# Kernel optimization log

Hardware: AMD Instinct MI355X
Metric: run time of the kernel (lower is better)

Reference implementation:

```python
import jax, jax.numpy as jnp
import numpy as np

N_NODES = 50000
N_EDGES = 1600000
E_DIM = 128
N_LAYERS = 3
N_GRAPHS = 32


def setup_inputs() -> dict:
    key = jax.random.key(0)
    ks = jax.random.split(key, 12)
    x = jax.random.normal(ks[0], (N_NODES,), dtype=jnp.float32)
    edge_index = jax.random.randint(ks[1], (2, N_EDGES), 0, N_NODES, dtype=jnp.int32)
    batch = jnp.sort(jax.random.randint(ks[2], (N_NODES,), 0, N_GRAPHS, dtype=jnp.int32))
    s_in = 1.0  # fan_in = 1 for the first linear
    s_e = 1.0 / np.sqrt(E_DIM)
    lin_w = jax.random.normal(ks[3], (1, E_DIM), jnp.float32) * s_in
    lin_b = jax.random.normal(ks[4], (E_DIM,), jnp.float32) * 0.01
    gcn_w = jax.random.normal(ks[5], (N_LAYERS, E_DIM, E_DIM), jnp.float32) * s_e
    gcn_b = jax.random.normal(ks[6], (N_LAYERS, E_DIM), jnp.float32) * 0.01
    r1_w = jax.random.normal(ks[7], (E_DIM, E_DIM), jnp.float32) * s_e
    r1_b = jax.random.normal(ks[8], (E_DIM,), jnp.float32) * 0.01
    r2_w = jax.random.normal(ks[9], (E_DIM, 1), jnp.float32) * s_e
    r2_b = jax.random.normal(ks[10], (1,), jnp.float32) * 0.01
    return {"x": x, "edge_index": edge_index, "batch": batch,
            "lin_w": lin_w, "lin_b": lin_b, "gcn_w": gcn_w, "gcn_b": gcn_b,
            "r1_w": r1_w, "r1_b": r1_b, "r2_w": r2_w, "r2_b": r2_b}


def reference(x, edge_index, batch, lin_w, lin_b, gcn_w, gcn_b, r1_w, r1_b, r2_w, r2_b):
    # input embedding: x.view(-1, 1) @ W + b -> [N, E]
    h = x.reshape(-1, 1) @ lin_w + lin_b

    # GCN normalization (add self-loops, symmetric deg^-1/2 norm) — structure is
    # identical across layers, so compute once.
    loops = jnp.arange(N_NODES, dtype=edge_index.dtype)
    src = jnp.concatenate([edge_index[0], loops])
    dst = jnp.concatenate([edge_index[1], loops])
    deg = jax.ops.segment_sum(jnp.ones(src.shape[0], h.dtype), dst, num_segments=N_NODES)
    dinv = jnp.where(deg > 0, jax.lax.rsqrt(deg), 0.0)
    norm = (dinv[src] * dinv[dst])[:, None]  # [E+N, 1]

    # NOTE: original calls x.relu() without assignment -> no activation (faithful).
    for l in range(N_LAYERS):
        h = h @ gcn_w[l]                                        # [N, E]
        h = jax.ops.segment_sum(h[src] * norm, dst, num_segments=N_NODES) + gcn_b[l]

    # global_add_pool over graphs
    pooled = jax.ops.segment_sum(h, batch, num_segments=N_GRAPHS)  # [G, E]
    hr = jnp.tanh(pooled @ r1_w + r1_b)
    return hr @ r2_w + r2_b  # [G, 1]
```

## Files before the change

kernel.cpp:

```cpp
#include <hip/hip_runtime.h>
#include <hip/hip_bf16.h>
#include <math.h>

#define NGRAPH 32
#define CAP 10240
#define EPT 24
#define EPB (256 * EPT)

__global__ void k_part(const int* __restrict__ src, const int* __restrict__ dst,
                       int* __restrict__ gcursor, unsigned int* __restrict__ packed, int E) {
    __shared__ unsigned int ldsbuf[EPB];
    __shared__ int hist[256], lofs[256], lcur[256], base[256];
    int tid = threadIdx.x;
    int e0 = blockIdx.x * EPB;
    hist[tid] = 0;
    __syncthreads();
    int d[EPT], s[EPT];
#pragma unroll
    for (int c = 0; c < EPT / 4; c++) {
        int e = e0 + c * 1024 + (tid << 2);
        if (e + 3 < E) {
            int4 dv = *(const int4*)&dst[e];
            int4 sv = *(const int4*)&src[e];
            d[4*c+0] = dv.x; d[4*c+1] = dv.y; d[4*c+2] = dv.z; d[4*c+3] = dv.w;
            s[4*c+0] = sv.x; s[4*c+1] = sv.y; s[4*c+2] = sv.z; s[4*c+3] = sv.w;
            atomicAdd(&hist[dv.x >> 8], 1);
            atomicAdd(&hist[dv.y >> 8], 1);
            atomicAdd(&hist[dv.z >> 8], 1);
            atomicAdd(&hist[dv.w >> 8], 1);
        } else {
#pragma unroll
            for (int k = 0; k < 4; k++) {
                int ee = e + k;
                if (ee < E) {
                    d[4*c+k] = dst[ee]; s[4*c+k] = src[ee];
                    atomicAdd(&hist[d[4*c+k] >> 8], 1);
                } else {
                    d[4*c+k] = -1;
                }
            }
        }
    }
    __syncthreads();
    int v = hist[tid];
    lofs[tid] = v;
    __syncthreads();
    for (int off = 1; off < 256; off <<= 1) {
        int t = (tid >= off) ? lofs[tid - off] : 0;
        __syncthreads();
        lofs[tid] += t;
        __syncthreads();
    }
    int total = lofs[255];
    int excl = lofs[tid] - v;
    lofs[tid] = excl;
    lcur[tid] = excl;
    if (v > 0) base[tid] = tid * CAP + atomicAdd(&gcursor[tid], v);
    __syncthreads();
#pragma unroll
    for (int c = 0; c < EPT; c++) {
        int dd = d[c];
        if (dd >= 0) {
            int bk = dd >> 8;
            int slot = atomicAdd(&lcur[bk], 1);
            ldsbuf[slot] = ((unsigned int)bk << 24) | ((unsigned int)s[c] << 8)
                         | (unsigned int)(dd & 255);
        }
    }
    __syncthreads();
    for (int i = tid; i < total; i += 256) {
        unsigned int w = ldsbuf[i];
        int bk = w >> 24;
        packed[base[bk] + (i - lofs[bk])] = w & 0xFFFFFFu;
    }
}

__global__ void k_bucket(const unsigned int* __restrict__ packed, const int* __restrict__ gcursor,
                         const float* __restrict__ x, const int* __restrict__ batch,
                         int* __restrict__ offs, int* __restrict__ deg,
                         float* __restrict__ dinv, float2* __restrict__ q0,
                         unsigned short* __restrict__ csr, float* __restrict__ S, int N) {
    __shared__ int cnt[256], lofs[256], lcur[256];
    __shared__ float cs[NGRAPH];
    int tid = threadIdx.x;
    int b = blockIdx.x;
    int start = b * CAP;
    int end = start + gcursor[b];
    cnt[tid] = 0;
    if (tid < NGRAPH) cs[tid] = 0.f;
    __syncthreads();
    for (int e = start + tid; e < end; e += 256)
        atomicAdd(&cnt[packed[e] & 255], 1);
    __syncthreads();
    int v = cnt[tid];
    int vp = (v + 1) & ~1;
    lofs[tid] = vp;
    __syncthreads();
    for (int off = 1; off < 256; off <<= 1) {
        int t = (tid >= off) ? lofs[tid - off] : 0;
        __syncthreads();
        lofs[tid] += t;
        __syncthreads();
    }
    int excl = lofs[tid] - vp;
    lcur[tid] = excl;
    int node = b * 256 + tid;
    if (node < N) {
        deg[node] = v;
        offs[node] = start + excl;
        float dv = rsqrtf((float)(v + 1));
        dinv[node] = dv;
        q0[node] = make_float2(x[node] * dv, dv);
        atomicAdd(&cs[batch[node]], 1.f);
    }
    __syncthreads();
    for (int e = start + tid; e < end; e += 256) {
        unsigned int p = packed[e];
        int pos = start + atomicAdd(&lcur[p & 255], 1);
        csr[pos] = (unsigned short)(p >> 8);
    }
    if (tid < NGRAPH && cs[tid] != 0.f) atomicAdd(&S[tid], cs[tid]);
}

template <int WRITE_Q>
__global__ void k_hop(const float2* __restrict__ qin, float2* __restrict__ outv,
                      const unsigned short* __restrict__ csr,
                      const int* __restrict__ offs, const int* __restrict__ deg,
                      const float* __restrict__ dinv, int N) {
    int tid = threadIdx.x;
    int lane = tid & 15;
    int node = blockIdx.x * 16 + (tid >> 4);
    if (node >= N) return;
    int e = offs[node], ne = deg[node];
    float sx = 0.0f, su = 0.0f;
    for (int j = 2 * lane; j < ne; j += 32) {
        ushort2 c = *(const ushort2*)&csr[e + j];
        float2 a = qin[c.x];
        sx += a.x; su += a.y;
        if (j + 1 < ne) {
            float2 b = qin[c.y];
            sx += b.x; su += b.y;
        }
    }
#pragma unroll
    for (int m = 8; m > 0; m >>= 1) {
        sx += __shfl_xor(sx, m);
        su += __shfl_xor(su, m);
    }
    if (lane == 0) {
        float2 qs = qin[node];
        float dv = dinv[node];
        float px = dv * (sx + qs.x), pu = dv * (su + qs.y);
        if (WRITE_Q) outv[node] = make_float2(px * dv, pu * dv);
        else         outv[node] = make_float2(px, pu);
    }
}

__global__ __launch_bounds__(1024) void k_chain(
        const float* __restrict__ lin_w, const float* __restrict__ lin_b,
        const float* __restrict__ gcn_w, const float* __restrict__ gcn_b,
        float* __restrict__ chainv) {
    __shared__ float W[128 * 128];
    __shared__ float v4[4 * 128];
    __shared__ float part[4 * 128 * 8];
    int tid = threadIdx.x;
    int j = tid & 127;
    int ch = tid >> 7;
    if (tid < 128) {
        v4[tid]       = lin_w[tid];
        v4[128 + tid] = lin_b[tid];
        v4[256 + tid] = gcn_b[tid];
        v4[384 + tid] = gcn_b[128 + tid];
    }
    for (int l = 0; l < 3; l++) {
        __syncthreads();
        const float4* Wg = (const float4*)(gcn_w + l * 128 * 128);
        float4* Ws = (float4*)W;
#pragma unroll
        for (int i = 0; i < 4; i++) Ws[tid + i * 1024] = Wg[tid + i * 1024];
        __syncthreads();
        float na = 0.f, nb = 0.f, nc = 0.f, nd = 0.f;
#pragma unroll
        for (int kk = 0; kk < 16; kk++) {
            int k = ch * 16 + kk;
            float w = W[k * 128 + j];
            na += v4[k] * w;
            nb += v4[128 + k] * w;
            nc += v4[256 + k] * w;
            nd += v4[384 + k] * w;
        }
        part[(0 * 128 + j) * 8 + ch] = na;
        part[(1 * 128 + j) * 8 + ch] = nb;
        part[(2 * 128 + j) * 8 + ch] = nc;
        part[(3 * 128 + j) * 8 + ch] = nd;
        __syncthreads();
        if (tid < 512) {
            int vec = tid >> 7, jj = tid & 127;
            float s = 0.f;
#pragma unroll
            for (int c = 0; c < 8; c++) s += part[(vec * 128 + jj) * 8 + c];
            if (vec < 2 || (vec == 2 && l >= 1) || (vec == 3 && l >= 2))
                v4[vec * 128 + jj] = s;
        }
    }
    __syncthreads();
    if (tid < 512) chainv[tid] = v4[tid];
}

__global__ __launch_bounds__(256) void k_mlp(
        const float* __restrict__ S, const float* __restrict__ chainv,
        const float2* __restrict__ q1, const float2* __restrict__ q2,
        const float2* __restrict__ p3, const float* __restrict__ dinv,
        const float* __restrict__ gcn_b,
        const float* __restrict__ r1_w, const float* __restrict__ r1_b,
        const float* __restrict__ r2_w, const float* __restrict__ r2_b,
        float* __restrict__ out, int N) {
    __shared__ float rw[128 * 128];
    __shared__ float pl[128], red[128];
    __shared__ float cnts[NGRAPH];
    __shared__ float r4[4 * 128];
    int tid = threadIdx.x;
    int g = blockIdx.x;
    {
        const float4* Rg = (const float4*)r1_w;
        float4* Rs = (float4*)rw;
#pragma unroll
        for (int i = 0; i < 16; i++) Rs[tid + i * 256] = Rg[tid + i * 256];
    }
    if (tid < NGRAPH) cnts[tid] = S[tid];
    __syncthreads();
    int r0 = 0;
    for (int i = 0; i < g; i++) r0 += (int)cnts[i];
    int cnt = (int)cnts[g];
    int r1 = r0 + cnt;
    float su1 = 0.f, su2 = 0.f, su3 = 0.f, sv3 = 0.f;
    for (int n = r0 + tid; n < r1; n += 256) {
        float inv = 1.0f / dinv[n];
        su1 += q1[n].y * inv;
        su2 += q2[n].y * inv;
        float2 p = p3[n];
        su3 += p.y; sv3 += p.x;
    }
#pragma unroll
    for (int m = 32; m > 0; m >>= 1) {
        su1 += __shfl_xor(su1, m);
        su2 += __shfl_xor(su2, m);
        su3 += __shfl_xor(su3, m);
        sv3 += __shfl_xor(sv3, m);
    }
    int wv = tid >> 6;
    if ((tid & 63) == 0) {
        r4[wv] = su1; r4[4 + wv] = su2; r4[8 + wv] = su3; r4[12 + wv] = sv3;
    }
    __syncthreads();
    su1 = r4[0] + r4[1] + r4[2] + r4[3];
    su2 = r4[4] + r4[5] + r4[6] + r4[7];
    su3 = r4[8] + r4[9] + r4[10] + r4[11];
    sv3 = r4[12] + r4[13] + r4[14] + r4[15];
    const float* b3 = gcn_b + 2 * 128;
    if (tid < 128)
        pl[tid] = sv3 * chainv[tid] + su3 * chainv[128 + tid] + su2 * chainv[256 + tid]
                + su1 * chainv[384 + tid] + (float)cnt * b3[tid];
    __syncthreads();
    int j = tid & 127, half = tid >> 7;
    float acc = 0.f;
#pragma unroll
    for (int kk = 0; kk < 64; kk++) {
        int k = half * 64 + kk;
        acc += pl[k] * rw[k * 128 + j];
    }
    r4[half * 128 + j] = acc;
    __syncthreads();
    if (tid < 128) {
        float a = r4[tid] + r4[128 + tid] + r1_b[tid];
        red[tid] = tanhf(a) * r2_w[tid];
    }
    __syncthreads();
    for (int sft = 64; sft > 0; sft >>= 1) {
        if (tid < sft) red[tid] += red[tid + sft];
        __syncthreads();
    }
    if (tid == 0) out[g] = red[0] + r2_b[0];
}

extern "C" void kernel_launch(void* const* d_in, const int* in_sizes, int n_in,
                              void* d_out, int out_size, void* d_ws, size_t ws_size,
                              hipStream_t stream) {
    const float* x     = (const float*)d_in[0];
    const int*   eidx  = (const int*)d_in[1];
    const int*   batch = (const int*)d_in[2];
    const float* lin_w = (const float*)d_in[3];
    const float* lin_b = (const float*)d_in[4];
    const float* gcn_w = (const float*)d_in[5];
    const float* gcn_b = (const float*)d_in[6];
    const float* r1_w  = (const float*)d_in[7];
    const float* r1_b  = (const float*)d_in[8];
    const float* r2_w  = (const float*)d_in[9];
    const float* r2_b  = (const float*)d_in[10];

    const int N = in_sizes[0];
    const int E = in_sizes[1] / 2;
    const int* src = eidx;
    const int* dst = eidx + E;
    const int NB = (N + 255) / 256;

    char* w = (char*)d_ws;
    float2* q0      = (float2*)w; w += (size_t)N * 8;
    float2* q1      = (float2*)w; w += (size_t)N * 8;
    float2* q2      = (float2*)w; w += (size_t)N * 8;
    float2* p3      = (float2*)w; w += (size_t)N * 8;
    unsigned int* packed = (unsigned int*)w; w += (size_t)256 * CAP * 4;
    int*    offs    = (int*)w;    w += (size_t)N * 4;
    int*    deg     = (int*)w;    w += (size_t)N * 4;
    float*  dinv    = (float*)w;  w += (size_t)N * 4;
    int*    gcursor = (int*)w;    w += 256 * 4;
    float*  S       = (float*)w;  w += 64 * 4;
    float*  chainv  = (float*)w;  w += 512 * 4;
    unsigned short* csr = (unsigned short*)w; w += (size_t)256 * CAP * 2 + 256;

    hipMemsetAsync(gcursor, 0, 256 * 4 + 64 * 4, stream);

    k_part<<<(E + EPB - 1) / EPB, 256, 0, stream>>>(src, dst, gcursor, packed, E);
    k_bucket<<<NB, 256, 0, stream>>>(packed, gcursor, x, batch, offs, deg, dinv, q0, csr, S, N);

    int hop_blocks = (N + 15) / 16;
    k_hop<1><<<hop_blocks, 256, 0, stream>>>(q0, q1, csr, offs, deg, dinv, N);
    k_hop<1><<<hop_blocks, 256, 0, stream>>>(q1, q2, csr, offs, deg, dinv, N);
    k_hop<0><<<hop_blocks, 256, 0, stream>>>(q2, p3, csr, offs, deg, dinv, N);

    k_chain<<<1, 1024, 0, stream>>>(lin_w, lin_b, gcn_w, gcn_b, chainv);
    k_mlp<<<NGRAPH, 256, 0, stream>>>(S, chainv, q1, q2, p3, dinv, gcn_b,
                                      r1_w, r1_b, r2_w, r2_b, (float*)d_out, N);
}
```

Baseline: 165.7 us.

## Fuse all stages into one cooperative persistent kernel with grid syncs

Replaces seven separate launches plus a memset with a single cooperative kernel of 256 blocks of 1024 threads. Stages are separated by grid.sync(): partitioning, bucketing/CSR build with the weight chain computed by a spare block, three hop passes looping over node tiles, and the per-graph MLP. The aim is to remove per-launch overhead and the gaps between small kernels. In exchange, each stage now runs on a fixed 256-block grid instead of a grid sized to its work, the weight matrices are read straight from global memory rather than staged in LDS, and every stage pays for a grid barrier.

```diff
diff --git a/kernel.cpp b/kernel.cpp
--- a/kernel.cpp
+++ b/kernel.cpp
@@ -1,286 +1,305 @@
 #include <hip/hip_runtime.h>
-#include <hip/hip_bf16.h>
+#include <hip/hip_cooperative_groups.h>
 #include <math.h>
+
+namespace cg = cooperative_groups;
 
 #define NGRAPH 32
 #define CAP 10240
-#define EPT 24
-#define EPB (256 * EPT)
-
-__global__ void k_part(const int* __restrict__ src, const int* __restrict__ dst,
-                       int* __restrict__ gcursor, unsigned int* __restrict__ packed, int E) {
+#define BT 1024
+#define GRID 256
+#define EPT 8
+#define EPB (BT * EPT)
+
+__global__ __launch_bounds__(BT, 4) void k_fused(
+    const int* __restrict__ src, const int* __restrict__ dst,
+    const float* __restrict__ x, const int* __restrict__ batch,
+    const float* __restrict__ lin_w, const float* __restrict__ lin_b,
+    const float* __restrict__ gcn_w, const float* __restrict__ gcn_b,
+    const float* __restrict__ r1_w, const float* __restrict__ r1_b,
+    const float* __restrict__ r2_w, const float* __restrict__ r2_b,
+    float* __restrict__ out,
+    unsigned int* __restrict__ packed, unsigned short* __restrict__ csr,
+    int* __restrict__ offs, int* __restrict__ deg,
+    float* __restrict__ dinv, float2* __restrict__ q0, float2* __restrict__ q1,
+    float2* __restrict__ q2, float2* __restrict__ p3,
+    int* __restrict__ gcursor, float* __restrict__ S, float* __restrict__ chainv,
+    int N, int E)
+{
+    cg::grid_group grid = cg::this_grid();
     __shared__ unsigned int ldsbuf[EPB];
-    __shared__ int hist[256], lofs[256], lcur[256], base[256];
-    int tid = threadIdx.x;
-    int e0 = blockIdx.x * EPB;
-    hist[tid] = 0;
-    __syncthreads();
-    int d[EPT], s[EPT];
-#pragma unroll
-    for (int c = 0; c < EPT / 4; c++) {
-        int e = e0 + c * 1024 + (tid << 2);
-        if (e + 3 < E) {
-            int4 dv = *(const int4*)&dst[e];
-            int4 sv = *(const int4*)&src[e];
-            d[4*c+0] = dv.x; d[4*c+1] = dv.y; d[4*c+2] = dv.z; d[4*c+3] = dv.w;
-            s[4*c+0] = sv.x; s[4*c+1] = sv.y; s[4*c+2] = sv.z; s[4*c+3] = sv.w;
-            atomicAdd(&hist[dv.x >> 8], 1);
-            atomicAdd(&hist[dv.y >> 8], 1);
-            atomicAdd(&hist[dv.z >> 8], 1);
-            atomicAdd(&hist[dv.w >> 8], 1);
-        } else {
-#pragma unroll
-            for (int k = 0; k < 4; k++) {
-                int ee = e + k;
-                if (ee < E) {
-                    d[4*c+k] = dst[ee]; s[4*c+k] = src[ee];
-                    atomicAdd(&hist[d[4*c+k] >> 8], 1);
-                } else {
-                    d[4*c+k] = -1;
+    __shared__ int h0[256], h1[256], h2[256], h3[256];
+    __shared__ float fbuf[640];
+
+    const int tid = threadIdx.x;
+    const int b = blockIdx.x;
+    const int NB = (N + 255) >> 8;
+    const int ntiles = (E + EPB - 1) / EPB;
+    const int nvb = (N + 63) >> 6;
+
+    if (b == 0) {
+        if (tid < 256) gcursor[tid] = 0;
+        else if (tid < 320) S[tid - 256] = 0.f;
+    }
+    grid.sync();
+
+    if (b < ntiles) {
+        int e0 = b * EPB;
+        if (tid < 256) h0[tid] = 0;
+        __syncthreads();
+        int d[EPT], s[EPT];
+#pragma unroll
+        for (int c = 0; c < EPT / 4; c++) {
+            int e = e0 + c * 4096 + (tid << 2);
+            if (e + 3 < E) {
+                int4 dv = *(const int4*)&dst[e];
+                int4 sv = *(const int4*)&src[e];
+                d[4*c+0] = dv.x; d[4*c+1] = dv.y; d[4*c+2] = dv.z; d[4*c+3] = dv.w;
+                s[4*c+0] = sv.x; s[4*c+1] = sv.y; s[4*c+2] = sv.z; s[4*c+3] = sv.w;
+                atomicAdd(&h0[dv.x >> 8], 1);
+                atomicAdd(&h0[dv.y >> 8], 1);
+                atomicAdd(&h0[dv.z >> 8], 1);
+                atomicAdd(&h0[dv.w >> 8], 1);
+            } else {
+#pragma unroll
+                for (int k = 0; k < 4; k++) {
+                    int ee = e + k;
+                    if (ee < E) {
+                        d[4*c+k] = dst[ee]; s[4*c+k] = src[ee];
+                        atomicAdd(&h0[d[4*c+k] >> 8], 1);
+                    } else {
+                        d[4*c+k] = -1;
+                    }
                 }
             }
         }
-    }
-    __syncthreads();
-    int v = hist[tid];
-    lofs[tid] = v;
-    __syncthreads();
-    for (int off = 1; off < 256; off <<= 1) {
-        int t = (tid >= off) ? lofs[tid - off] : 0;
-        __syncthreads();
-        lofs[tid] += t;
-        __syncthreads();
-    }
-    int total = lofs[255];
-    int excl = lofs[tid] - v;
-    lofs[tid] = excl;
-    lcur[tid] = excl;
-    if (v > 0) base[tid] = tid * CAP + atomicAdd(&gcursor[tid], v);
-    __syncthreads();
-#pragma unroll
-    for (int c = 0; c < EPT; c++) {
-        int dd = d[c];
-        if (dd >= 0) {
-            int bk = dd >> 8;
-            int slot = atomicAdd(&lcur[bk], 1);
-            ldsbuf[slot] = ((unsigned int)bk << 24) | ((unsigned int)s[c] << 8)
-                         | (unsigned int)(dd & 255);
-        }
-    }
-    __syncthreads();
-    for (int i = tid; i < total; i += 256) {
-        unsigned int w = ldsbuf[i];
-        int bk = w >> 24;
-        packed[base[bk] + (i - lofs[bk])] = w & 0xFFFFFFu;
-    }
-}
-
-__global__ void k_bucket(const unsigned int* __restrict__ packed, const int* __restrict__ gcursor,
-                         const float* __restrict__ x, const int* __restrict__ batch,
-                         int* __restrict__ offs, int* __restrict__ deg,
-                         float* __restrict__ dinv, float2* __restrict__ q0,
-                         unsigned short* __restrict__ csr, float* __restrict__ S, int N) {
-    __shared__ int cnt[256], lofs[256], lcur[256];
-    __shared__ float cs[NGRAPH];
-    int tid = threadIdx.x;
-    int b = blockIdx.x;
-    int start = b * CAP;
-    int end = start + gcursor[b];
-    cnt[tid] = 0;
-    if (tid < NGRAPH) cs[tid] = 0.f;
-    __syncthreads();
-    for (int e = start + tid; e < end; e += 256)
-        atomicAdd(&cnt[packed[e] & 255], 1);
-    __syncthreads();
-    int v = cnt[tid];
-    int vp = (v + 1) & ~1;
-    lofs[tid] = vp;
-    __syncthreads();
-    for (int off = 1; off < 256; off <<= 1) {
-        int t = (tid >= off) ? lofs[tid - off] : 0;
-        __syncthreads();
-        lofs[tid] += t;
-        __syncthreads();
-    }
-    int excl = lofs[tid] - vp;
-    lcur[tid] = excl;
-    int node = b * 256 + tid;
-    if (node < N) {
-        deg[node] = v;
-        offs[node] = start + excl;
-        float dv = rsqrtf((float)(v + 1));
-        dinv[node] = dv;
-        q0[node] = make_float2(x[node] * dv, dv);
-        atomicAdd(&cs[batch[node]], 1.f);
-    }
-    __syncthreads();
-    for (int e = start + tid; e < end; e += 256) {
-        unsigned int p = packed[e];
-        int pos = start + atomicAdd(&lcur[p & 255], 1);
-        csr[pos] = (unsigned short)(p >> 8);
-    }
-    if (tid < NGRAPH && cs[tid] != 0.f) atomicAdd(&S[tid], cs[tid]);
-}
-
-template <int WRITE_Q>
-__global__ void k_hop(const float2* __restrict__ qin, float2* __restrict__ outv,
-                      const unsigned short* __restrict__ csr,
-                      const int* __restrict__ offs, const int* __restrict__ deg,
-                      const float* __restrict__ dinv, int N) {
-    int tid = threadIdx.x;
-    int lane = tid & 15;
-    int node = blockIdx.x * 16 + (tid >> 4);
-    if (node >= N) return;
-    int e = offs[node], ne = deg[node];
-    float sx = 0.0f, su = 0.0f;
-    for (int j = 2 * lane; j < ne; j += 32) {
-        ushort2 c = *(const ushort2*)&csr[e + j];
-        float2 a = qin[c.x];
-        sx += a.x; su += a.y;
-        if (j + 1 < ne) {
-            float2 b = qin[c.y];
-            sx += b.x; su += b.y;
-        }
-    }
-#pragma unroll
-    for (int m = 8; m > 0; m >>= 1) {
-        sx += __shfl_xor(sx, m);
-        su += __shfl_xor(su, m);
-    }
-    if (lane == 0) {
-        float2 qs = qin[node];
-        float dv = dinv[node];
-        float px = dv * (sx + qs.x), pu = dv * (su + qs.y);
-        if (WRITE_Q) outv[node] = make_float2(px * dv, pu * dv);
-        else         outv[node] = make_float2(px, pu);
-    }
-}
-
-__global__ __launch_bounds__(1024) void k_chain(
-        const float* __restrict__ lin_w, const float* __restrict__ lin_b,
-        const float* __restrict__ gcn_w, const float* __restrict__ gcn_b,
-        float* __restrict__ chainv) {
-    __shared__ float W[128 * 128];
-    __shared__ float v4[4 * 128];
-    __shared__ float part[4 * 128 * 8];
-    int tid = threadIdx.x;
-    int j = tid & 127;
-    int ch = tid >> 7;
-    if (tid < 128) {
-        v4[tid]       = lin_w[tid];
-        v4[128 + tid] = lin_b[tid];
-        v4[256 + tid] = gcn_b[tid];
-        v4[384 + tid] = gcn_b[128 + tid];
-    }
+        __syncthreads();
+        int v = 0;
+        if (tid < 256) { v = h0[tid]; h1[tid] = v; }
+        __syncthreads();
+        for (int off = 1; off < 256; off <<= 1) {
+            int t = 0;
+            if (tid < 256 && tid >= off) t = h1[tid - off];
+            __syncthreads();
+            if (tid < 256) h1[tid] += t;
+            __syncthreads();
+        }
+        int total = h1[255];
+        __syncthreads();
+        if (tid < 256) {
+            int excl = h1[tid] - v;
+            h1[tid] = excl;
+            h2[tid] = excl;
+            if (v > 0) h3[tid] = tid * CAP + atomicAdd(&gcursor[tid], v);
+        }
+        __syncthreads();
+#pragma unroll
+        for (int c = 0; c < EPT; c++) {
+            int dd = d[c];
+            if (dd >= 0) {
+                int bk = dd >> 8;
+                int slot = atomicAdd(&h2[bk], 1);
+                ldsbuf[slot] = ((unsigned int)bk << 24) | ((unsigned int)s[c] << 8)
+                             | (unsigned int)(dd & 255);
+            }
+        }
+        __syncthreads();
+        for (int i = tid; i < total; i += BT) {
+            unsigned int wv = ldsbuf[i];
+            int bk = wv >> 24;
+            packed[h3[bk] + (i - h1[bk])] = wv & 0xFFFFFFu;
+        }
+    }
+    grid.sync();
+
+    if (b < NB) {
+        int start = b * CAP;
+        int end = start + gcursor[b];
+        if (tid < 256) h0[tid] = 0;
+        if (tid < NGRAPH) fbuf[tid] = 0.f;
+        __syncthreads();
+        for (int e = start + tid; e < end; e += BT)
+            atomicAdd(&h0[packed[e] & 255], 1);
+        __syncthreads();
+        int v = 0, vp = 0;
+        if (tid < 256) {
+            v = h0[tid];
+            vp = (v + 1) & ~1;
+            h1[tid] = vp;
+        }
+        __syncthreads();
+        for (int off = 1; off < 256; off <<= 1) {
+            int t = 0;
+            if (tid < 256 && tid >= off) t = h1[tid - off];
+            __syncthreads();
+            if (tid < 256) h1[tid] += t;
+            __syncthreads();
+        }
+        if (tid < 256) {
+            int excl = h1[tid] - vp;
+            h2[tid] = excl;
+            int node = b * 256 + tid;
+            if (node < N) {
+                deg[node] = v;
+                offs[node] = start + excl;
+                float dv = rsqrtf((float)(v + 1));
+                dinv[node] = dv;
+                q0[node] = make_float2(x[node] * dv, dv);
+                atomicAdd(&fbuf[batch[node]], 1.f);
+            }
+        }
+        __syncthreads();
+        for (int e = start + tid; e < end; e += BT) {
+            unsigned int p = packed[e];
+            int pos = start + atomicAdd(&h2[p & 255], 1);
+            csr[pos] = (unsigned short)(p >> 8);
+        }
+        if (tid < NGRAPH && fbuf[tid] != 0.f) atomicAdd(&S[tid], fbuf[tid]);
+    } else if (b == NB) {
+        float* v4 = fbuf;
+        float* ch = (float*)ldsbuf;
+        if (tid < 128) {
+            v4[tid]       = lin_w[tid];
+            v4[128 + tid] = lin_b[tid];
+            v4[256 + tid] = gcn_b[tid];
+            v4[384 + tid] = gcn_b[128 + tid];
+        }
+        int j = tid & 127, kh = tid >> 7;
+        for (int l = 0; l < 3; l++) {
+            __syncthreads();
+            const float* W = gcn_w + l * 128 * 128;
+            float na = 0.f, nb = 0.f, nc = 0.f, nd = 0.f;
+#pragma unroll
+            for (int kk = 0; kk < 16; kk++) {
+                int k = kh * 16 + kk;
+                float w = W[k * 128 + j];
+                na += v4[k] * w;
+                nb += v4[128 + k] * w;
+                nc += v4[256 + k] * w;
+                nd += v4[384 + k] * w;
+            }
+            ch[(0 * 128 + j) * 8 + kh] = na;
+            ch[(1 * 128 + j) * 8 + kh] = nb;
+            ch[(2 * 128 + j) * 8 + kh] = nc;
+            ch[(3 * 128 + j) * 8 + kh] = nd;
+            __syncthreads();
+            if (tid < 512) {
+                int vec = tid >> 7, jj = tid & 127;
+                float s = 0.f;
+#pragma unroll
+                for (int c = 0; c < 8; c++) s += ch[(vec * 128 + jj) * 8 + c];
+                if (vec < 2 || (vec == 2 && l >= 1) || (vec == 3 && l >= 2))
+                    v4[vec * 128 + jj] = s;
+            }
+        }
+        __syncthreads();
+        if (tid < 512) chainv[tid] = v4[tid];
+    }
+    grid.sync();
+
+#pragma unroll
     for (int l = 0; l < 3; l++) {
-        __syncthreads();
-        const float4* Wg = (const float4*)(gcn_w + l * 128 * 128);
-        float4* Ws = (float4*)W;
-#pragma unroll
-        for (int i = 0; i < 4; i++) Ws[tid + i * 1024] = Wg[tid + i * 1024];
-        __syncthreads();
-        float na = 0.f, nb = 0.f, nc = 0.f, nd = 0.f;
+        const float2* qin = (l == 0) ? q0 : (l == 1) ? q1 : q2;
+        float2* outv      = (l == 0) ? q1 : (l == 1) ? q2 : p3;
+        int lane = tid & 15;
+        int sub = tid >> 4;
+        for (int vb = b; vb < nvb; vb += GRID) {
+            int node = vb * 64 + sub;
+            if (node < N) {
+                int e = offs[node], ne = deg[node];
+                float sx = 0.f, su = 0.f;
+                for (int j = 2 * lane; j < ne; j += 32) {
+                    ushort2 c = *(const ushort2*)&csr[e + j];
+                    float2 a = qin[c.x];
+                    sx += a.x; su += a.y;
+                    if (j + 1 < ne) {
+                        float2 bb = qin[c.y];
+                        sx += bb.x; su += bb.y;
+                    }
+                }
+#pragma unroll
+                for (int m = 8; m > 0; m >>= 1) {
+                    sx += __shfl_xor(sx, m);
+                    su += __shfl_xor(su, m);
+                }
+                if (lane == 0) {
+                    float2 qs = qin[node];
+                    float dv = dinv[node];
+                    float px = dv * (sx + qs.x), pu = dv * (su + qs.y);
+                    if (l < 2) outv[node] = make_float2(px * dv, pu * dv);
+                    else       outv[node] = make_float2(px, pu);
+                }
+            }
+        }
+        grid.sync();
+    }
+
+    if (b < NGRAPH) {
+        int g = b;
+        float* f    = (float*)ldsbuf;
+        float* cnts = f;
+        float* rsum = f + 32;
+        float* pl   = f + 96;
+        float* mm   = f + 224;
+        float* red  = f + 1248;
+        if (tid < NGRAPH) cnts[tid] = S[tid];
+        __syncthreads();
+        int r0 = 0;
+        for (int i = 0; i < g; i++) r0 += (int)cnts[i];
+        int cnt = (int)cnts[g];
+        int r1 = r0 + cnt;
+        float su1 = 0.f, su2 = 0.f, su3 = 0.f, sv3 = 0.f;
+        for (int n = r0 + tid; n < r1; n += BT) {
+            float inv = 1.0f / dinv[n];
+            su1 += q1[n].y * inv;
+            su2 += q2[n].y * inv;
+            float2 p = p3[n];
+            su3 += p.y; sv3 += p.x;
+        }
+#pragma unroll
+        for (int m = 32; m > 0; m >>= 1) {
+            su1 += __shfl_xor(su1, m);
+            su2 += __shfl_xor(su2, m);
+            su3 += __shfl_xor(su3, m);
+            sv3 += __shfl_xor(sv3, m);
+        }
+        int wv = tid >> 6;
+        if ((tid & 63) == 0) {
+            rsum[wv] = su1; rsum[16 + wv] = su2; rsum[32 + wv] = su3; rsum[48 + wv] = sv3;
+        }
+        __syncthreads();
+        su1 = 0.f; su2 = 0.f; su3 = 0.f; sv3 = 0.f;
+#pragma unroll
+        for (int i = 0; i < 16; i++) {
+            su1 += rsum[i]; su2 += rsum[16 + i]; su3 += rsum[32 + i]; sv3 += rsum[48 + i];
+        }
+        const float* b3 = gcn_b + 2 * 128;
+        if (tid < 128)
+            pl[tid] = sv3 * chainv[tid] + su3 * chainv[128 + tid] + su2 * chainv[256 + tid]
+                    + su1 * chainv[384 + tid] + (float)cnt * b3[tid];
+        __syncthreads();
+        int j = tid & 127, ck = tid >> 7;
+        float acc = 0.f;
 #pragma unroll
         for (int kk = 0; kk < 16; kk++) {
-            int k = ch * 16 + kk;
-            float w = W[k * 128 + j];
-            na += v4[k] * w;
-            nb += v4[128 + k] * w;
-            nc += v4[256 + k] * w;
-            nd += v4[384 + k] * w;
-        }
-        part[(0 * 128 + j) * 8 + ch] = na;
-        part[(1 * 128 + j) * 8 + ch] = nb;
-        part[(2 * 128 + j) * 8 + ch] = nc;
-        part[(3 * 128 + j) * 8 + ch] = nd;
-        __syncthreads();
-        if (tid < 512) {
-            int vec = tid >> 7, jj = tid & 127;
-            float s = 0.f;
-#pragma unroll
-            for (int c = 0; c < 8; c++) s += part[(vec * 128 + jj) * 8 + c];
-            if (vec < 2 || (vec == 2 && l >= 1) || (vec == 3 && l >= 2))
-                v4[vec * 128 + jj] = s;
-        }
-    }
-    __syncthreads();
-    if (tid < 512) chainv[tid] = v4[tid];
-}
-
-__global__ __launch_bounds__(256) void k_mlp(
-        const float* __restrict__ S, const float* __restrict__ chainv,
-        const float2* __restrict__ q1, const float2* __restrict__ q2,
-        const float2* __restrict__ p3, const float* __restrict__ dinv,
-        const float* __restrict__ gcn_b,
-        const float* __restrict__ r1_w, const float* __restrict__ r1_b,
-        const float* __restrict__ r2_w, const float* __restrict__ r2_b,
-        float* __restrict__ out, int N) {
-    __shared__ float rw[128 * 128];
-    __shared__ float pl[128], red[128];
-    __shared__ float cnts[NGRAPH];
-    __shared__ float r4[4 * 128];
-    int tid = threadIdx.x;
-    int g = blockIdx.x;
-    {
-        const float4* Rg = (const float4*)r1_w;
-        float4* Rs = (float4*)rw;
-#pragma unroll
-        for (int i = 0; i < 16; i++) Rs[tid + i * 256] = Rg[tid + i * 256];
-    }
-    if (tid < NGRAPH) cnts[tid] = S[tid];
-    __syncthreads();
-    int r0 = 0;
-    for (int i = 0; i < g; i++) r0 += (int)cnts[i];
-    int cnt = (int)cnts[g];
-    int r1 = r0 + cnt;
-    float su1 = 0.f, su2 = 0.f, su3 = 0.f, sv3 = 0.f;
-    for (int n = r0 + tid; n < r1; n += 256) {
-        float inv = 1.0f / dinv[n];
-        su1 += q1[n].y * inv;
-        su2 += q2[n].y * inv;
-        float2 p = p3[n];
-        su3 += p.y; sv3 += p.x;
-    }
-#pragma unroll
-    for (int m = 32; m > 0; m >>= 1) {
-        su1 += __shfl_xor(su1, m);
-        su2 += __shfl_xor(su2, m);
-        su3 += __shfl_xor(su3, m);
-        sv3 += __shfl_xor(sv3, m);
-    }
-    int wv = tid >> 6;
-    if ((tid & 63) == 0) {
-        r4[wv] = su1; r4[4 + wv] = su2; r4[8 + wv] = su3; r4[12 + wv] = sv3;
-    }
-    __syncthreads();
-    su1 = r4[0] + r4[1] + r4[2] + r4[3];
-    su2 = r4[4] + r4[5] + r4[6] + r4[7];
-    su3 = r4[8] + r4[9] + r4[10] + r4[11];
-    sv3 = r4[12] + r4[13] + r4[14] + r4[15];
-    const float* b3 = gcn_b + 2 * 128;
-    if (tid < 128)
-        pl[tid] = sv3 * chainv[tid] + su3 * chainv[128 + tid] + su2 * chainv[256 + tid]
-                + su1 * chainv[384 + tid] + (float)cnt * b3[tid];
-    __syncthreads();
-    int j = tid & 127, half = tid >> 7;
-    float acc = 0.f;
-#pragma unroll
-    for (int kk = 0; kk < 64; kk++) {
-        int k = half * 64 + kk;
-        acc += pl[k] * rw[k * 128 + j];
-    }
-    r4[half * 128 + j] = acc;
-    __syncthreads();
-    if (tid < 128) {
-        float a = r4[tid] + r4[128 + tid] + r1_b[tid];
-        red[tid] = tanhf(a) * r2_w[tid];
-    }
-    __syncthreads();
-    for (int sft = 64; sft > 0; sft >>= 1) {
-        if (tid < sft) red[tid] += red[tid + sft];
-        __syncthreads();
-    }
-    if (tid == 0) out[g] = red[0] + r2_b[0];
+            int k = ck * 16 + kk;
+            acc += pl[k] * r1_w[k * 128 + j];
+        }
+        mm[ck * 128 + j] = acc;
+        __syncthreads();
+        if (tid < 128) {
+            float a = r1_b[tid];
+#pragma unroll
+            for (int c = 0; c < 8; c++) a += mm[c * 128 + tid];
+            red[tid] = tanhf(a) * r2_w[tid];
+        }
+        __syncthreads();
+        for (int sft = 64; sft > 0; sft >>= 1) {
+            if (tid < sft) red[tid] += red[tid + sft];
+            __syncthreads();
+        }
+        if (tid == 0) out[g] = red[0] + r2_b[0];
+    }
 }
 
 extern "C" void kernel_launch(void* const* d_in, const int* in_sizes, int n_in,
@@ -298,11 +317,10 @@
     const float* r2_w  = (const float*)d_in[9];
     const float* r2_b  = (const float*)d_in[10];
 
-    const int N = in_sizes[0];
-    const int E = in_sizes[1] / 2;
+    int N = in_sizes[0];
+    int E = in_sizes[1] / 2;
     const int* src = eidx;
     const int* dst = eidx + E;
-    const int NB = (N + 255) / 256;
 
     char* w = (char*)d_ws;
     float2* q0      = (float2*)w; w += (size_t)N * 8;
@@ -318,17 +336,18 @@
     float*  chainv  = (float*)w;  w += 512 * 4;
     unsigned short* csr = (unsigned short*)w; w += (size_t)256 * CAP * 2 + 256;
 
-    hipMemsetAsync(gcursor, 0, 256 * 4 + 64 * 4, stream);
-
-    k_part<<<(E + EPB - 1) / EPB, 256, 0, stream>>>(src, dst, gcursor, packed, E);
-    k_bucket<<<NB, 256, 0, stream>>>(packed, gcursor, x, batch, offs, deg, dinv, q0, csr, S, N);
-
-    int hop_blocks = (N + 15) / 16;
-    k_hop<1><<<hop_blocks, 256, 0, stream>>>(q0, q1, csr, offs, deg, dinv, N);
-    k_hop<1><<<hop_blocks, 256, 0, stream>>>(q1, q2, csr, offs, deg, dinv, N);
-    k_hop<0><<<hop_blocks, 256, 0, stream>>>(q2, p3, csr, offs, deg, dinv, N);
-
-    k_chain<<<1, 1024, 0, stream>>>(lin_w, lin_b, gcn_w, gcn_b, chainv);
-    k_mlp<<<NGRAPH, 256, 0, stream>>>(S, chainv, q1, q2, p3, dinv, gcn_b,
-                                      r1_w, r1_b, r2_w, r2_b, (float*)d_out, N);
+    float* outp = (float*)d_out;
+
+    void* args[] = {
+        (void*)&src, (void*)&dst, (void*)&x, (void*)&batch,
+        (void*)&lin_w, (void*)&lin_b, (void*)&gcn_w, (void*)&gcn_b,
+        (void*)&r1_w, (void*)&r1_b, (void*)&r2_w, (void*)&r2_b,
+        (void*)&outp, (void*)&packed, (void*)&csr,
+        (void*)&offs, (void*)&deg, (void*)&dinv,
+        (void*)&q0, (void*)&q1, (void*)&q2, (void*)&p3,
+        (void*)&gcursor, (void*)&S, (void*)&chainv,
+        (void*)&N, (void*)&E
+    };
+    hipLaunchCooperativeKernel((const void*)k_fused, dim3(GRID), dim3(BT),
+                               args, 0, stream);
 }
```

Measured after the change: 331.2 us. 99.8% more time.
